# Kernel optimization log

Measured on AMD Instinct MI355X. Metric: run time of the kernel, lower is better.

The kernel has to match this reference:

```python
import jax, jax.numpy as jnp
import numpy as np

B, S, DIM = 2, 4096, 1024
H, HD = 16, 64          # num_heads, head_dim (DIM = H*HD)
KN = 64                 # k neighbors per query
SCALE = 1.0 / np.sqrt(HD)
CANTOR_DEPTH = 8


def _cantor_coords(seq_len: int, depth: int = CANTOR_DEPTH) -> np.ndarray:
    """Vectorized replica of CantorAttention._compute_cantor_coord."""
    x = np.arange(seq_len, dtype=np.float64) / max(1, seq_len - 1)
    x = np.clip(x, 1e-06, 1.0 - 1e-06)
    val = np.zeros(seq_len, dtype=np.float64)
    factor = 0.5
    for _ in range(depth):
        xs = x * 3.0
        digit = np.floor(xs)
        x = xs - digit
        val += factor * (digit == 2)
        factor *= 0.5
    return val.astype(np.float32)


def _build_routes(seq_len: int, k: int) -> np.ndarray:
    coords = _cantor_coords(seq_len)
    dist = np.abs(coords[:, None] - coords[None, :])  # [S, S]
    routes = np.argsort(dist, axis=1, kind='stable')[:, :k]  # k smallest
    return routes.astype(np.int32)


def setup_inputs() -> dict:
    key = jax.random.key(0)
    kx, kw1, kb1, kw2, kb2 = jax.random.split(key, 5)
    x = jax.random.normal(kx, (B, S, DIM), dtype=jnp.float32)
    # learned params (qkv and out projections)
    W_qkv = jax.random.normal(kw1, (DIM, 3 * DIM), dtype=jnp.float32) * (1.0 / np.sqrt(DIM))
    b_qkv = jax.random.normal(kb1, (3 * DIM,), dtype=jnp.float32) * 0.01
    W_out = jax.random.normal(kw2, (DIM, DIM), dtype=jnp.float32) * (1.0 / np.sqrt(DIM))
    b_out = jax.random.normal(kb2, (DIM,), dtype=jnp.float32) * 0.01
    routes = jnp.asarray(_build_routes(S, KN))  # [S, KN] int32, positional Cantor kNN
    return {"x": x, "W_qkv": W_qkv, "b_qkv": b_qkv, "W_out": W_out, "b_out": b_out, "routes": routes}


def reference(x, W_qkv, b_qkv, W_out, b_out, routes):
    Bs, Sl, _ = x.shape
    qkv = x @ W_qkv + b_qkv                                   # [B,S,3*DIM]
    qkv = qkv.reshape(Bs, Sl, 3, H, HD).transpose(2, 0, 3, 1, 4)
    q, k, v = qkv[0], qkv[1], qkv[2]                          # [B,H,S,HD]
    k_g = k[:, :, routes, :]                                  # [B,H,S,KN,HD]
    v_g = v[:, :, routes, :]                                  # [B,H,S,KN,HD]
    scores = jnp.einsum('bhqd,bhqkd->bhqk', q, k_g) * SCALE   # [B,H,S,KN]
    attn = jax.nn.softmax(scores, axis=-1)
    out = jnp.einsum('bhqk,bhqkd->bhqd', attn, v_g)           # [B,H,S,HD]
    out = out.transpose(0, 2, 1, 3).reshape(Bs, Sl, DIM)
    return out @ W_out + b_out
```

## Files before the change

kernel.cpp:

```cpp
#include <hip/hip_runtime.h>
#include <hip/hip_bf16.h>
#include <stdint.h>

#define DEVI __device__ __forceinline__

typedef __bf16 bf16x8 __attribute__((ext_vector_type(8)));
typedef float f32x4 __attribute__((ext_vector_type(4)));
typedef unsigned short ushort8v __attribute__((ext_vector_type(8)));

static constexpr int SEQ = 4096;
static constexpr int DIM_ = 1024;
static constexpr int NH = 16;
static constexpr int HD_ = 64;
static constexpr float SCALE_ = 0.125f;

DEVI unsigned short f2bf(float f) {
  __hip_bfloat16 h = __float2bfloat16(f);
  return __builtin_bit_cast(unsigned short, h);
}


__global__ void k_cvt_bf16(const float* __restrict__ in, unsigned short* __restrict__ out) {
  int i = (blockIdx.x * 256 + threadIdx.x) * 4;
  float4 v = *reinterpret_cast<const float4*>(in + i);
  ushort4 o;
  o.x = f2bf(v.x); o.y = f2bf(v.y); o.z = f2bf(v.z); o.w = f2bf(v.w);
  *reinterpret_cast<ushort4*>(out + i) = o;
}

__global__ void k_transpose_cvt(const float* __restrict__ in, unsigned short* __restrict__ out,
                                int K, int N) {
  __shared__ float tile[64][65];
  const int n0 = blockIdx.x * 64, k0 = blockIdx.y * 64;
  const int tr = threadIdx.x >> 6, tc = threadIdx.x & 63;
#pragma unroll
  for (int p = 0; p < 16; ++p) {
    int r = p * 4 + tr;
    tile[r][tc] = in[(size_t)(k0 + r) * N + n0 + tc];
  }
  __syncthreads();
#pragma unroll
  for (int p = 0; p < 16; ++p) {
    int r = p * 4 + tr;
    out[(size_t)(n0 + r) * K + k0 + tc] = f2bf(tile[tc][r]);
  }
}


DEVI void load16_lds(const void* g, void* l) {
  __builtin_amdgcn_global_load_lds((__attribute__((address_space(1))) void*)(g),
                                   (__attribute__((address_space(3))) void*)(l),
                                   16, 0, 0);
}

template <int MODE>
__global__ __launch_bounds__(256, 2)
void k_gemm_bt(const unsigned short* __restrict__ A,
               const unsigned short* __restrict__ Bt,
               const float* __restrict__ bias,
               float* __restrict__ outF,
               unsigned short* __restrict__ outQ,
               unsigned short* __restrict__ outK,
               unsigned short* __restrict__ outV,
               int M, int N, int K) {
  constexpr int BK = 32;
  __shared__ alignas(16) unsigned short As[128 * BK];
  __shared__ alignas(16) unsigned short Bs[128 * BK];
  const int tid = threadIdx.x;
  const int wave = tid >> 6, lane = tid & 63;
  const int wr = wave >> 1, wc = wave & 1;
  const int bm = blockIdx.x * 128, bn = blockIdx.y * 128;

  f32x4 acc[4][4] = {};

  const int srow = lane >> 2;
  const int scol = (lane & 3) * 8;
  const unsigned short* aS0 = A + (size_t)(bm + wave * 16 + srow) * K + scol;
  const unsigned short* aS1 = aS0 + (size_t)64 * K;
  const unsigned short* bS0 = Bt + (size_t)(bn + wave * 16 + srow) * K + scol;
  const unsigned short* bS1 = bS0 + (size_t)64 * K;
  unsigned short* aD0 = &As[(wave * 16) * BK];
  unsigned short* aD1 = &As[(64 + wave * 16) * BK];
  unsigned short* bD0 = &Bs[(wave * 16) * BK];
  unsigned short* bD1 = &Bs[(64 + wave * 16) * BK];

  const unsigned short* aRd = &As[(wr * 64 + (lane & 15)) * BK + (lane >> 4) * 8];
  const unsigned short* bRd = &Bs[(wc * 64 + (lane & 15)) * BK + (lane >> 4) * 8];

  for (int k0 = 0; k0 < K; k0 += BK) {
    load16_lds(aS0 + k0, aD0);
    load16_lds(aS1 + k0, aD1);
    load16_lds(bS0 + k0, bD0);
    load16_lds(bS1 + k0, bD1);
    __syncthreads();

    bf16x8 af[4], bfr[4];
#pragma unroll
    for (int m = 0; m < 4; ++m)
      af[m] = *reinterpret_cast<const bf16x8*>(aRd + m * 16 * BK);
#pragma unroll
    for (int n = 0; n < 4; ++n)
      bfr[n] = *reinterpret_cast<const bf16x8*>(bRd + n * 16 * BK);
#pragma unroll
    for (int m = 0; m < 4; ++m)
#pragma unroll
      for (int n = 0; n < 4; ++n)
        acc[m][n] = __builtin_amdgcn_mfma_f32_16x16x32_bf16(af[m], bfr[n], acc[m][n], 0, 0, 0);
    __syncthreads();
  }

  const int r0 = (lane >> 4) * 4;
  const int c0 = lane & 15;
#pragma unroll
  for (int m = 0; m < 4; ++m) {
#pragma unroll
    for (int n = 0; n < 4; ++n) {
      const int col = bn + wc * 64 + n * 16 + c0;
      const float bv = bias[col];
#pragma unroll
      for (int j = 0; j < 4; ++j) {
        const int row = bm + wr * 64 + m * 16 + r0 + j;
        const float v = acc[m][n][j] + bv;
        if constexpr (MODE == 0) {
          outF[(size_t)row * N + col] = v;
        } else {
          const int t = col >> 10;
          const int hh = (col >> 6) & 15;
          const int d = col & 63;
          const int b = row >> 12;
          const int s = row & 4095;
          unsigned short* dst = (t == 0) ? outQ : (t == 1) ? outK : outV;
          dst[((size_t)(b * NH + hh) * SEQ + s) * HD_ + d] = f2bf(v);
        }
      }
    }
  }
}


__global__ void k_gid(const int* __restrict__ routes, int* __restrict__ gid, int* __restrict__ cnt) {
  const int s = blockIdx.x * 256 + threadIdx.x;
  const int lead = routes[s * 64];
  int g = s;
  if (lead >= 0 && lead < SEQ && lead != s) {
    bool eq = true;
    const int4* a = reinterpret_cast<const int4*>(routes + (size_t)s * 64);
    const int4* b = reinterpret_cast<const int4*>(routes + (size_t)lead * 64);
#pragma unroll
    for (int i = 0; i < 16; ++i) {
      int4 x = a[i], y = b[i];
      eq = eq && (x.x == y.x) && (x.y == y.y) && (x.z == y.z) && (x.w == y.w);
    }
    if (eq) g = lead;
  }
  gid[s] = g;
  atomicAdd(&cnt[g], 1);
}

__global__ void k_tilebase(const int* __restrict__ cnt, int* __restrict__ tileBase,
                           int* __restrict__ nTiles) {
  const int g = blockIdx.x * 256 + threadIdx.x;
  const int c = cnt[g];
  if (c > 0) {
    tileBase[g] = atomicAdd(nTiles, (c + 15) >> 4);
  }
}

__global__ void k_scatter(const int* __restrict__ gid, const int* __restrict__ tileBase,
                          int* __restrict__ pos, int* __restrict__ tileQ,
                          int* __restrict__ tileLead) {
  const int s = blockIdx.x * 256 + threadIdx.x;
  const int g = gid[s];
  const int p = atomicAdd(&pos[g], 1);
  const int tile = tileBase[g] + (p >> 4);
  tileQ[tile * 16 + (p & 15)] = s;
  if ((p & 15) == 0) tileLead[tile] = g;
}


__global__ __launch_bounds__(256)
void k_attn_grp(const unsigned short* __restrict__ Q,
                const unsigned short* __restrict__ Kb,
                const unsigned short* __restrict__ Vb,
                const int* __restrict__ routes,
                const int* __restrict__ tileQ,
                const int* __restrict__ tileLead,
                const int* __restrict__ nTilesPtr,
                unsigned short* __restrict__ att) {
  const int tile = blockIdx.x;
  if (tile >= *nTilesPtr) return;

  __shared__ int sMemRaw[16];
  __shared__ int sMemEff[16];
  __shared__ int sRoutes[64];
  __shared__ alignas(16) unsigned short sKV[4][4096];
  __shared__ alignas(16) unsigned short sP[4][16 * 72];

  const int tid = threadIdx.x;
  if (tid < 16) {
    const int v = tileQ[tile * 16 + tid];
    const int v0 = tileQ[tile * 16];
    sMemRaw[tid] = v;
    sMemEff[tid] = (v < 0) ? v0 : v;
  } else if (tid >= 64 && tid < 128) {
    const int lead = tileLead[tile];
    sRoutes[tid - 64] = routes[(size_t)lead * 64 + (tid - 64)];
  }
  __syncthreads();

  const int wave = tid >> 6, lane = tid & 63;
  unsigned short* KV = sKV[wave];
  unsigned short* P = sP[wave];
  const int hi = lane >> 4;
  const int l15 = lane & 15;
  const int l7 = lane & 7;
  const int rr = lane >> 3;

#pragma unroll 1
  for (int ih = 0; ih < 2; ++ih) {
    const int bh = blockIdx.y * 8 + wave * 2 + ih;
    const size_t base = (size_t)bh * (SEQ * HD_);

    __builtin_amdgcn_s_waitcnt(0);
    __builtin_amdgcn_sched_barrier(0);

    {
      const int sc = ((l7 - rr) & 7) * 8;
#pragma unroll
      for (int t = 0; t < 8; ++t) {
        const int rk = sRoutes[t * 8 + rr];
        load16_lds(Kb + base + (size_t)rk * HD_ + sc, &KV[t * 512]);
      }
    }

    bf16x8 qa0, qa1;
    {
      const unsigned short* qrow = Q + base + (size_t)sMemEff[l15] * HD_ + hi * 8;
      qa0 = *reinterpret_cast<const bf16x8*>(qrow);
      qa1 = *reinterpret_cast<const bf16x8*>(qrow + 32);
    }
    __builtin_amdgcn_s_waitcnt(0);
    __builtin_amdgcn_sched_barrier(0);

    f32x4 accS[4] = {};
#pragma unroll
    for (int nb = 0; nb < 4; ++nb) {
      const int key = nb * 16 + l15;
      const int rot = 8 * (key & 7);
      const int ae0 = key * 64 + (((hi * 8) + rot) & 63);
      const int ae1 = key * 64 + (((32 + hi * 8) + rot) & 63);
      bf16x8 kf0 = *reinterpret_cast<const bf16x8*>(&KV[ae0]);
      bf16x8 kf1 = *reinterpret_cast<const bf16x8*>(&KV[ae1]);
      accS[nb] = __builtin_amdgcn_mfma_f32_16x16x32_bf16(qa0, kf0, accS[nb], 0, 0, 0);
      accS[nb] = __builtin_amdgcn_mfma_f32_16x16x32_bf16(qa1, kf1, accS[nb], 0, 0, 0);
    }

#pragma unroll
    for (int jj = 0; jj < 4; ++jj) {
      float m = fmaxf(fmaxf(accS[0][jj], accS[1][jj]), fmaxf(accS[2][jj], accS[3][jj]));
#pragma unroll
      for (int o = 1; o < 16; o <<= 1) m = fmaxf(m, __shfl_xor(m, o));
      const float e0 = __expf((accS[0][jj] - m) * SCALE_);
      const float e1 = __expf((accS[1][jj] - m) * SCALE_);
      const float e2 = __expf((accS[2][jj] - m) * SCALE_);
      const float e3 = __expf((accS[3][jj] - m) * SCALE_);
      float sum = (e0 + e1) + (e2 + e3);
#pragma unroll
      for (int o = 1; o < 16; o <<= 1) sum += __shfl_xor(sum, o);
      const float rs = __builtin_amdgcn_rcpf(sum);
      const int row = hi * 4 + jj;
      P[row * 72 + 0 + l15] = f2bf(e0 * rs);
      P[row * 72 + 16 + l15] = f2bf(e1 * rs);
      P[row * 72 + 32 + l15] = f2bf(e2 * rs);
      P[row * 72 + 48 + l15] = f2bf(e3 * rs);
    }

    asm volatile("s_waitcnt lgkmcnt(0)" ::: "memory");
    __builtin_amdgcn_sched_barrier(0);
    {
#pragma unroll
      for (int t = 0; t < 8; ++t) {
        const int rk = sRoutes[t * 8 + rr];
        const int sc = ((l7 - 2 * (t & 3)) & 7) * 8;
        load16_lds(Vb + base + (size_t)rk * HD_ + sc, &KV[t * 512]);
      }
    }
    __builtin_amdgcn_s_waitcnt(0);
    __builtin_amdgcn_sched_barrier(0);

    f32x4 accO[4] = {};
#pragma unroll
    for (int ks = 0; ks < 2; ++ks) {
      bf16x8 pf = *reinterpret_cast<const bf16x8*>(&P[l15 * 72 + ks * 32 + hi * 8]);
#pragma unroll
      for (int nb = 0; nb < 4; ++nb) {
        const int d = nb * 16 + l15;
        const int rot = (d + 16 * hi) & 63;
        bf16x8 vf;
#pragma unroll
        for (int j = 0; j < 8; ++j) {
          const int k = ks * 32 + hi * 8 + j;
          vf[j] = *reinterpret_cast<const __bf16*>(&KV[k * 64 + rot]);
        }
        accO[nb] = __builtin_amdgcn_mfma_f32_16x16x32_bf16(pf, vf, accO[nb], 0, 0, 0);
      }
    }

    const int b = bh >> 4, h = bh & 15;
#pragma unroll
    for (int jj = 0; jj < 4; ++jj) {
      const int sQ = sMemRaw[hi * 4 + jj];
      if (sQ >= 0) {
#pragma unroll
        for (int nb = 0; nb < 4; ++nb) {
          att[((size_t)(b * SEQ + sQ)) * DIM_ + h * HD_ + nb * 16 + l15] = f2bf(accO[nb][jj]);
        }
      }
    }
  }
}


extern "C" void kernel_launch(void* const* d_in, const int* in_sizes, int n_in,
                              void* d_out, int out_size, void* d_ws, size_t ws_size,
                              hipStream_t stream) {
  (void)in_sizes; (void)n_in; (void)out_size; (void)ws_size;
  const float* x      = (const float*)d_in[0];
  const float* Wqkv   = (const float*)d_in[1];
  const float* bqkv   = (const float*)d_in[2];
  const float* Wout   = (const float*)d_in[3];
  const float* bout   = (const float*)d_in[4];
  const int*   routes = (const int*)d_in[5];
  float* out = (float*)d_out;

  uint8_t* ws = (uint8_t*)d_ws;
  unsigned short* wqkvT = (unsigned short*)(ws);
  unsigned short* woutT = (unsigned short*)(ws + 6291456);
  unsigned short* Qb    = (unsigned short*)(ws + 8388608);
  unsigned short* Kb    = (unsigned short*)(ws + 25165824);
  unsigned short* Vb    = (unsigned short*)(ws + 41943040);
  unsigned short* att   = (unsigned short*)(ws + 58720256);

  unsigned short* xb = (unsigned short*)d_out;
  uint8_t* g0 = (uint8_t*)d_out + (16u << 20);
  int* gidArr   = (int*)(g0);
  int* cnt      = (int*)(g0 + 16384);
  int* pos      = (int*)(g0 + 32768);
  int* tileBase = (int*)(g0 + 49152);
  int* nTiles   = (int*)(g0 + 65536);
  int* tileLead = (int*)(g0 + 81920);
  int* tileQ    = (int*)(g0 + 98304);

  hipMemsetAsync(cnt, 0, 16384, stream);
  hipMemsetAsync(pos, 0, 16384, stream);
  hipMemsetAsync(nTiles, 0, 4, stream);
  hipMemsetAsync(tileQ, 0xFF, 4096 * 16 * 4, stream);

  k_gid<<<16, 256, 0, stream>>>(routes, gidArr, cnt);
  k_tilebase<<<16, 256, 0, stream>>>(cnt, tileBase, nTiles);
  k_scatter<<<16, 256, 0, stream>>>(gidArr, tileBase, pos, tileQ, tileLead);

  k_cvt_bf16<<<8192, 256, 0, stream>>>(x, xb);
  k_transpose_cvt<<<dim3(48, 16), 256, 0, stream>>>(Wqkv, wqkvT, 1024, 3072);
  k_transpose_cvt<<<dim3(16, 16), 256, 0, stream>>>(Wout, woutT, 1024, 1024);
  k_gemm_bt<1><<<dim3(64, 24), 256, 0, stream>>>(xb, wqkvT, bqkv, nullptr, Qb, Kb, Vb,
                                                 8192, 3072, 1024);
  k_attn_grp<<<dim3(4096, 4), 256, 0, stream>>>(Qb, Kb, Vb, routes, tileQ, tileLead,
                                                nTiles, att);
  k_gemm_bt<0><<<dim3(64, 8), 256, 0, stream>>>(att, woutT, bout, out,
                                                nullptr, nullptr, nullptr, 8192, 1024, 1024);
}
```

Measured before the change: 172.6 us.

## Rewrite GEMMs as 256x256 tiles with 4-stage LDS pipeline and swizzle

Replaces the 128x128, single-buffered GEMM with a 256x256-tile, 512-thread kernel. It uses a 4-deep LDS ring buffer fed by async global_load_lds, with vmcnt waits replacing the double syncthreads. It also XOR-swizzles the LDS layout to avoid bank conflicts, remaps workgroup IDs for L2 locality, and raises MFMA priority with s_setprio. The aim is to hide global-load latency and increase reuse per tile. The trade-offs are higher register pressure from 32 accumulators per lane and fewer workgroups (128 for the out projection), which may underfill the GPU.

```diff
diff --git a/kernel.cpp b/kernel.cpp
--- a/kernel.cpp
+++ b/kernel.cpp
@@ -54,8 +54,8 @@
 }
 
 template <int MODE>
-__global__ __launch_bounds__(256, 2)
-void k_gemm_bt(const unsigned short* __restrict__ A,
+__global__ __launch_bounds__(512, 2)
+void k_gemm256(const unsigned short* __restrict__ A,
                const unsigned short* __restrict__ Bt,
                const float* __restrict__ bias,
                float* __restrict__ outF,
@@ -63,63 +63,92 @@
                unsigned short* __restrict__ outK,
                unsigned short* __restrict__ outV,
                int M, int N, int K) {
-  constexpr int BK = 32;
-  __shared__ alignas(16) unsigned short As[128 * BK];
-  __shared__ alignas(16) unsigned short Bs[128 * BK];
+  __shared__ alignas(16) unsigned short As[4][8192];
+  __shared__ alignas(16) unsigned short Bs[4][8192];
+
   const int tid = threadIdx.x;
   const int wave = tid >> 6, lane = tid & 63;
-  const int wr = wave >> 1, wc = wave & 1;
-  const int bm = blockIdx.x * 128, bn = blockIdx.y * 128;
-
-  f32x4 acc[4][4] = {};
-
-  const int srow = lane >> 2;
-  const int scol = (lane & 3) * 8;
-  const unsigned short* aS0 = A + (size_t)(bm + wave * 16 + srow) * K + scol;
-  const unsigned short* aS1 = aS0 + (size_t)64 * K;
-  const unsigned short* bS0 = Bt + (size_t)(bn + wave * 16 + srow) * K + scol;
-  const unsigned short* bS1 = bS0 + (size_t)64 * K;
-  unsigned short* aD0 = &As[(wave * 16) * BK];
-  unsigned short* aD1 = &As[(64 + wave * 16) * BK];
-  unsigned short* bD0 = &Bs[(wave * 16) * BK];
-  unsigned short* bD1 = &Bs[(64 + wave * 16) * BK];
-
-  const unsigned short* aRd = &As[(wr * 64 + (lane & 15)) * BK + (lane >> 4) * 8];
-  const unsigned short* bRd = &Bs[(wc * 64 + (lane & 15)) * BK + (lane >> 4) * 8];
-
-  for (int k0 = 0; k0 < K; k0 += BK) {
-    load16_lds(aS0 + k0, aD0);
-    load16_lds(aS1 + k0, aD1);
-    load16_lds(bS0 + k0, bD0);
-    load16_lds(bS1 + k0, bD1);
-    __syncthreads();
-
-    bf16x8 af[4], bfr[4];
-#pragma unroll
-    for (int m = 0; m < 4; ++m)
-      af[m] = *reinterpret_cast<const bf16x8*>(aRd + m * 16 * BK);
+  const int wr = wave >> 2, wc = wave & 3;
+  const int l15 = lane & 15, q = lane >> 4;
+
+  const int gm = M >> 8;
+  const int gn = N >> 8;
+  const int nwg = gm * gn;
+  int wg = blockIdx.y * gridDim.x + blockIdx.x;
+  wg = (wg & 7) * (nwg >> 3) + (wg >> 3);
+  const int bm = (wg % gm) * 256;
+  const int bn = (wg / gm) * 256;
+
+  const int NT = K >> 5;
+
+  const int c8 = (lane & 3) ^ ((lane >> 3) & 3);
+  const int r0 = wave * 32 + (lane >> 2);
+  const unsigned short* aG0 = A + (size_t)(bm + r0) * K + c8 * 8;
+  const unsigned short* aG1 = A + (size_t)(bm + r0 + 16) * K + c8 * 8;
+  const unsigned short* bG0 = Bt + (size_t)(bn + r0) * K + c8 * 8;
+  const unsigned short* bG1 = Bt + (size_t)(bn + r0 + 16) * K + c8 * 8;
+  const int ldsOff = wave * 1024;
+
+  const int sw = (q ^ ((l15 >> 1) & 3)) << 4;
+  const int aRdByte = (wr * 128 + l15) * 64 + sw;
+  const int bRdByte = (wc * 64 + l15) * 64 + sw;
+
+  f32x4 acc[8][4] = {};
+
+#pragma unroll
+  for (int t = 0; t < 3; ++t) {
+    const int kk = t * 32;
+    load16_lds(aG0 + kk, &As[t][ldsOff]);
+    load16_lds(aG1 + kk, &As[t][ldsOff + 512]);
+    load16_lds(bG0 + kk, &Bs[t][ldsOff]);
+    load16_lds(bG1 + kk, &Bs[t][ldsOff + 512]);
+  }
+
+#pragma unroll 1
+  for (int t = 0; t < NT; ++t) {
+    asm volatile("s_waitcnt vmcnt(8)" ::: "memory");
+    __builtin_amdgcn_s_barrier();
+
+    {
+      const int tt = (t + 3 < NT) ? (t + 3) : t;
+      const int kk = tt * 32;
+      const int s3 = (t + 3) & 3;
+      load16_lds(aG0 + kk, &As[s3][ldsOff]);
+      load16_lds(aG1 + kk, &As[s3][ldsOff + 512]);
+      load16_lds(bG0 + kk, &Bs[s3][ldsOff]);
+      load16_lds(bG1 + kk, &Bs[s3][ldsOff + 512]);
+    }
+
+    const int s = t & 3;
+    const char* aB = reinterpret_cast<const char*>(&As[s][0]) + aRdByte;
+    const char* bB = reinterpret_cast<const char*>(&Bs[s][0]) + bRdByte;
+    bf16x8 bfr[4], af[8];
 #pragma unroll
     for (int n = 0; n < 4; ++n)
-      bfr[n] = *reinterpret_cast<const bf16x8*>(bRd + n * 16 * BK);
-#pragma unroll
-    for (int m = 0; m < 4; ++m)
+      bfr[n] = *reinterpret_cast<const bf16x8*>(bB + n * 1024);
+#pragma unroll
+    for (int m = 0; m < 8; ++m)
+      af[m] = *reinterpret_cast<const bf16x8*>(aB + m * 1024);
+
+    __builtin_amdgcn_s_setprio(1);
+#pragma unroll
+    for (int m = 0; m < 8; ++m)
 #pragma unroll
       for (int n = 0; n < 4; ++n)
         acc[m][n] = __builtin_amdgcn_mfma_f32_16x16x32_bf16(af[m], bfr[n], acc[m][n], 0, 0, 0);
-    __syncthreads();
-  }
-
-  const int r0 = (lane >> 4) * 4;
-  const int c0 = lane & 15;
-#pragma unroll
-  for (int m = 0; m < 4; ++m) {
+    __builtin_amdgcn_s_setprio(0);
+  }
+
+  const int fr0 = q * 4;
+#pragma unroll
+  for (int m = 0; m < 8; ++m) {
 #pragma unroll
     for (int n = 0; n < 4; ++n) {
-      const int col = bn + wc * 64 + n * 16 + c0;
+      const int col = bn + wc * 64 + n * 16 + l15;
       const float bv = bias[col];
 #pragma unroll
       for (int j = 0; j < 4; ++j) {
-        const int row = bm + wr * 64 + m * 16 + r0 + j;
+        const int row = bm + wr * 128 + m * 16 + fr0 + j;
         const float v = acc[m][n][j] + bv;
         if constexpr (MODE == 0) {
           outF[(size_t)row * N + col] = v;
@@ -128,9 +157,9 @@
           const int hh = (col >> 6) & 15;
           const int d = col & 63;
           const int b = row >> 12;
-          const int s = row & 4095;
+          const int ss = row & 4095;
           unsigned short* dst = (t == 0) ? outQ : (t == 1) ? outK : outV;
-          dst[((size_t)(b * NH + hh) * SEQ + s) * HD_ + d] = f2bf(v);
+          dst[((size_t)(b * NH + hh) * SEQ + ss) * HD_ + d] = f2bf(v);
         }
       }
     }
@@ -363,10 +392,11 @@
   k_cvt_bf16<<<8192, 256, 0, stream>>>(x, xb);
   k_transpose_cvt<<<dim3(48, 16), 256, 0, stream>>>(Wqkv, wqkvT, 1024, 3072);
   k_transpose_cvt<<<dim3(16, 16), 256, 0, stream>>>(Wout, woutT, 1024, 1024);
-  k_gemm_bt<1><<<dim3(64, 24), 256, 0, stream>>>(xb, wqkvT, bqkv, nullptr, Qb, Kb, Vb,
+
+  k_gemm256<1><<<dim3(32, 12), 512, 0, stream>>>(xb, wqkvT, bqkv, nullptr, Qb, Kb, Vb,
                                                  8192, 3072, 1024);
   k_attn_grp<<<dim3(4096, 4), 256, 0, stream>>>(Qb, Kb, Vb, routes, tileQ, tileLead,
                                                 nTiles, att);
-  k_gemm_bt<0><<<dim3(64, 8), 256, 0, stream>>>(att, woutT, bout, out,
+  k_gemm256<0><<<dim3(32, 4), 512, 0, stream>>>(att, woutT, bout, out,
                                                 nullptr, nullptr, nullptr, 8192, 1024, 1024);
 }
```

After: 207.7 us. +20.4%, slower.
